# Optimization experiments

Hardware: AMD Instinct MI355X
Metric: run time of the kernel (lower is better)

## Reference

```python
import jax, jax.numpy as jnp
import numpy as np

RHO = 10.0
TAU = 0.1


def setup_inputs() -> dict:
    key = jax.random.key(0)
    k1, k2 = jax.random.split(key)
    N, D, C = 8192, 512, 128
    embeddings = jax.random.normal(k1, (N, D), dtype=jnp.float32)
    classes = jax.random.randint(k2, (N,), 0, C, dtype=jnp.int64)
    return {"embeddings": embeddings, "classes": classes}


def reference(embeddings, classes):
    n = embeddings.shape[0]
    dt = embeddings.dtype

    # calculate_similarities_pt: cosine similarity (dot products of L2-normalized embeddings)
    norms = jnp.linalg.norm(embeddings, axis=1, keepdims=True)
    normed = embeddings / jnp.maximum(norms, jnp.asarray(1e-12, dt))
    dot_products = jnp.einsum("nd,md->nm", normed, normed)  # [N, N]

    # calculate_groups_pt: same-class mask (excluding self) and different-class mask
    eq = classes[:, None] == classes[None, :]
    eye = jnp.eye(n, dtype=bool)
    same_group = (eq & ~eye).astype(dt)       # [N, N]
    different_group = (~eq).astype(dt)        # [N, N]

    # diagonal gets factor -RHO -> strongly negative score, effectively masked out
    raw_scores = ((same_group + different_group) * (1.0 + RHO) - RHO) * dot_products / TAU
    max_raw_score = jnp.max(raw_scores, axis=1, keepdims=True)
    shifted_scores = jnp.exp(raw_scores - max_raw_score)

    shifted_positive_scores = same_group * shifted_scores
    sum_shifted_negative_scores = jnp.sum(different_group * shifted_scores, axis=1, keepdims=True)

    denom = shifted_positive_scores + sum_shifted_negative_scores
    # safe_division: 0 where denominator is 0
    ratio = jnp.where(denom > 0, shifted_positive_scores / jnp.where(denom > 0, denom, 1.0), 0.0)
    # safe_log: 0 where argument is 0 (masked by same_group anyway)
    log_ratio = jnp.where(ratio > 0, jnp.log(jnp.where(ratio > 0, ratio, 1.0)), 0.0)
    infonce_losses = -log_ratio * same_group

    num_pos = jnp.sum(same_group)
    loss = jnp.where(num_pos > 0, jnp.sum(infonce_losses) / jnp.where(num_pos > 0, num_pos, 1.0), 0.0)
    return loss
```

## Files before the change

kernel.cpp:

```cpp
#include <hip/hip_runtime.h>
#include <hip/hip_bf16.h>


constexpr int   D      = 512;
constexpr int   BT     = 128;
constexpr float SHIFTL = 14.4269504088896340f;
constexpr float QS2L   = 10.0f * 1.4426950408889634f / 16129.0f;
constexpr float LN2    = 0.6931471805599453f;

typedef __attribute__((ext_vector_type(4))) int i32x4;
typedef unsigned char uchar;
typedef unsigned long ulong_t;

__device__ inline void gload_lds16(const uchar* g, void* l) {
    __builtin_amdgcn_global_load_lds(
        (const __attribute__((address_space(1))) void*)g,
        (__attribute__((address_space(3))) void*)l, 16, 0, 0);
}

__global__ void k_normalize(const float* __restrict__ emb,
                            const int* __restrict__ classes,
                            uchar* __restrict__ normed,
                            int* __restrict__ hist, int n) {
    if (blockIdx.x == 0) {
        __shared__ int h[128];
        if (threadIdx.x < 128) h[threadIdx.x] = 0;
        __syncthreads();
        for (int i = threadIdx.x; i < n; i += 256)
            atomicAdd(&h[classes[i] & 127], 1);
        __syncthreads();
        if (threadIdx.x < 128) hist[threadIdx.x] = h[threadIdx.x];
    }
    int row  = blockIdx.x * 4 + (threadIdx.x >> 6);
    int lane = threadIdx.x & 63;
    if (row >= n) return;
    const float4* src = (const float4*)(emb + (size_t)row * D);
    float4 a = src[lane * 2];
    float4 b = src[lane * 2 + 1];
    float ss = a.x*a.x + a.y*a.y + a.z*a.z + a.w*a.w
             + b.x*b.x + b.y*b.y + b.z*b.z + b.w*b.w;
#pragma unroll
    for (int m = 1; m < 64; m <<= 1) ss += __shfl_xor(ss, m, 64);
    float sc = 127.0f / fmaxf(sqrtf(ss), 1e-12f);
    union { signed char c[8]; ulong_t u; } o;
    float v[8] = {a.x, a.y, a.z, a.w, b.x, b.y, b.z, b.w};
#pragma unroll
    for (int k = 0; k < 8; ++k) {
        int q = (int)rintf(v[k] * sc);
        q = q > 127 ? 127 : (q < -127 ? -127 : q);
        o.c[k] = (signed char)q;
    }
    *(ulong_t*)&normed[(size_t)row * D + lane * 8] = o.u;
}

__global__ __launch_bounds__(256, 2) void k_zgemm(
    const uchar* __restrict__ normed, const int* __restrict__ classes,
    float* __restrict__ Zpart, int n, int nb, int npairs) {
    __shared__ char Blds[65536];
    __shared__ int clsrow[BT], clscol[BT];

    const int tid  = threadIdx.x;
    const int lane = tid & 63;
    const int w    = tid >> 6;
    const int l15  = lane & 15, l4 = lane >> 4;
    const size_t QS = (size_t)64 * n;

    int q8 = npairs >> 3, r8 = npairs & 7;
    int xcd = blockIdx.x & 7, off = blockIdx.x >> 3;
    int orig = (xcd < r8 ? xcd * (q8 + 1) : r8 * (q8 + 1) + (xcd - r8) * q8) + off;

    const int sgrid = nb >> 3;
    int idx = orig, si = 0;
    for (;;) { int rc = 36 + (sgrid - 1 - si) * 64; if (idx < rc) break; idx -= rc; ++si; }
    int bi, bj;
    if (idx < 36) { int u = 0, rem = 8; while (idx >= rem) { idx -= rem; ++u; --rem; }
                    bi = si * 8 + u; bj = si * 8 + u + idx; }
    else { idx -= 36; int sj = si + 1 + (idx >> 6); int v = idx & 63;
           bi = si * 8 + (v >> 3); bj = sj * 8 + (v & 7); }
    const int row0 = bi * BT, c0 = bj * BT;
    const bool diagblk = (bi == bj);

    if (tid < BT) clsrow[tid] = classes[row0 + tid];
    else          clscol[tid - BT] = classes[c0 + tid - BT];

    int crow[2][4];
#pragma unroll
    for (int rg = 0; rg < 2; ++rg)
#pragma unroll
        for (int r = 0; r < 4; ++r)
            crow[rg][r] = classes[row0 + w * 32 + rg * 16 + l4 * 4 + r];
    int ccv[8];
#pragma unroll
    for (int cf = 0; cf < 8; ++cf)
        ccv[cf] = classes[c0 + cf * 16 + l15];

    i32x4 areg[2][8];
#pragma unroll
    for (int rg = 0; rg < 2; ++rg)
#pragma unroll
        for (int kf = 0; kf < 8; ++kf)
            areg[rg][kf] = *(const i32x4*)&normed[
                (size_t)(row0 + w * 32 + rg * 16 + l15) * D + kf * 64 + l4 * 16];

    {
        const int colw = w * 2 + (lane >> 5);
        const int p    = lane & 31;
#pragma unroll
        for (int rr = 0; rr < 16; ++rr) {
            int col = rr * 8 + colw;
            gload_lds16(&normed[(size_t)(c0 + col) * D + ((p ^ (col & 7)) << 4)],
                        Blds + (rr * 8 + w * 2) * 512 + lane * 16);
        }
    }
    __syncthreads();

    i32x4 acc[2][8];
#pragma unroll
    for (int rg = 0; rg < 2; ++rg)
#pragma unroll
        for (int cf = 0; cf < 8; ++cf) acc[rg][cf] = (i32x4){0, 0, 0, 0};

    const int csw = l15 & 7;
#pragma unroll
    for (int kf = 0; kf < 8; ++kf) {
#pragma unroll
        for (int cf = 0; cf < 8; ++cf) {
            int cc = cf * 16 + l15;
            i32x4 bf = *(const i32x4*)(Blds + cc * 512 +
                        (((kf * 4 + l4) ^ csw) << 4));
            acc[0][cf] = __builtin_amdgcn_mfma_i32_16x16x64_i8(
                areg[0][kf], bf, acc[0][cf], 0, 0, 0);
            acc[1][cf] = __builtin_amdgcn_mfma_i32_16x16x64_i8(
                areg[1][kf], bf, acc[1][cf], 0, 0, 0);
        }
    }
    __syncthreads();

    float* redc = (float*)Blds;
    float* redr = (float*)(Blds + 8192);

    float cq[8][3];
#pragma unroll
    for (int cf = 0; cf < 8; ++cf) cq[cf][0] = cq[cf][1] = cq[cf][2] = 0.f;

#pragma unroll
    for (int rg = 0; rg < 2; ++rg) {
#pragma unroll
        for (int r = 0; r < 4; ++r) {
            int rr = w * 32 + rg * 16 + l4 * 4 + r;
            int cr = crow[rg][r];
            float z = 0.f, ns = 0.f, p1 = 0.f;
#pragma unroll
            for (int cf = 0; cf < 8; ++cf) {
                int cc = cf * 16 + l15;
                float tt = fmaf((float)acc[rg][cf][r], QS2L, -SHIFTL);
                float e = exp2f(tt);
                bool same = (cr == ccv[cf]);
                bool dg   = diagblk && (rr == cc);
                if (!same) { z += e; cq[cf][0] += e; }
                else if (!dg) { ns += tt; p1 += e; cq[cf][1] += tt; cq[cf][2] += e; }
            }
#pragma unroll
            for (int m = 1; m < 16; m <<= 1) {
                z  += __shfl_xor(z,  m, 16);
                ns += __shfl_xor(ns, m, 16);
                p1 += __shfl_xor(p1, m, 16);
            }
            if (l15 == 0) {
                redr[rr * 3 + 0] = z;
                redr[rr * 3 + 1] = ns;
                redr[rr * 3 + 2] = p1;
            }
        }
    }
    if (!diagblk) {
#pragma unroll
        for (int cf = 0; cf < 8; ++cf) {
            float z = cq[cf][0], nsv = cq[cf][1], p = cq[cf][2];
            z += __shfl_xor(z, 16, 64);  z += __shfl_xor(z, 32, 64);
            nsv += __shfl_xor(nsv, 16, 64); nsv += __shfl_xor(nsv, 32, 64);
            p += __shfl_xor(p, 16, 64);  p += __shfl_xor(p, 32, 64);
            if (l4 == 0) {
                float* pp = &redc[(w * 128 + cf * 16 + l15) * 3];
                pp[0] = z; pp[1] = nsv; pp[2] = p;
            }
        }
    }
    __syncthreads();

    if (tid < BT) {
#pragma unroll
        for (int q = 0; q < 3; ++q)
            Zpart[q * QS + (size_t)bj * n + row0 + tid] = redr[tid * 3 + q];
    } else if (!diagblk) {
        int cc = tid - BT;
#pragma unroll
        for (int q = 0; q < 3; ++q)
            Zpart[q * QS + (size_t)bi * n + c0 + cc] =
                redc[(0 * 128 + cc) * 3 + q] + redc[(1 * 128 + cc) * 3 + q] +
                redc[(2 * 128 + cc) * 3 + q] + redc[(3 * 128 + cc) * 3 + q];
    }
}

__global__ void k_rowterms(const float* __restrict__ Zpart,
                           const int* __restrict__ classes,
                           const int* __restrict__ hist,
                           float* __restrict__ rowloss,
                           float* __restrict__ rowcnt, int n) {
    int i = blockIdx.x * 256 + threadIdx.x;
    if (i >= n) return;
    const size_t QS = (size_t)64 * n;
    float z = 0.f, ns = 0.f, p1 = 0.f;
    for (int s = 0; s < 64; ++s) {
        size_t o = (size_t)s * n + i;
        z  += Zpart[o];
        ns += Zpart[QS + o];
        p1 += Zpart[2 * QS + o];
    }
    float c = (float)(hist[classes[i] & 127] - 1);
    rowloss[i] = -ns * LN2 + c * logf(z) + p1 / z;
    rowcnt[i]  = c;
}

__global__ void k_final(const float* __restrict__ rowloss,
                        const float* __restrict__ rowcnt,
                        float* __restrict__ out, int n) {
    __shared__ float sl[1024];
    __shared__ float sc[1024];
    float l = 0.f, c = 0.f;
    for (int i = threadIdx.x; i < n; i += 1024) {
        l += rowloss[i];
        c += rowcnt[i];
    }
    sl[threadIdx.x] = l;
    sc[threadIdx.x] = c;
    __syncthreads();
    for (int s = 512; s > 0; s >>= 1) {
        if (threadIdx.x < s) {
            sl[threadIdx.x] += sl[threadIdx.x + s];
            sc[threadIdx.x] += sc[threadIdx.x + s];
        }
        __syncthreads();
    }
    if (threadIdx.x == 0)
        out[0] = (sc[0] > 0.f) ? sl[0] / sc[0] : 0.f;
}

extern "C" void kernel_launch(void* const* d_in, const int* in_sizes, int n_in,
                              void* d_out, int out_size, void* d_ws, size_t ws_size,
                              hipStream_t stream) {
    const float* emb     = (const float*)d_in[0];
    const int*   classes = (const int*)d_in[1];
    float*       out     = (float*)d_out;
    const int n  = in_sizes[1];
    const int nb = n / BT;
    const int npairs = nb * (nb + 1) / 2;

    uchar*  normed  = (uchar*)d_ws;
    float*  Zpart   = (float*)((char*)d_ws + (size_t)n * D);
    float*  rowloss = Zpart + (size_t)3 * 64 * n;
    float*  rowcnt  = rowloss + n;
    int*    hist    = (int*)(rowcnt + n);

    k_normalize<<<n / 4, 256, 0, stream>>>(emb, classes, normed, hist, n);
    k_zgemm<<<npairs, 256, 0, stream>>>(normed, classes, Zpart, n, nb, npairs);
    k_rowterms<<<(n + 255) / 256, 256, 0, stream>>>(Zpart, classes, hist, rowloss, rowcnt, n);
    k_final<<<1, 1024, 0, stream>>>(rowloss, rowcnt, out, n);
}
```

Measured before the change: 86.46 us.

## Pipeline B-tile loads through a triple-buffered LDS ring over K

Replaces the single 64KB LDS load of the full B tile (all of K) with a 3-slot 16KB ring that streams K in 128-byte steps. The next stages are prefetched with async global-to-LDS loads while MFMAs run, with vmcnt waits and barriers between steps and raised wave priority around the MFMA bursts. The smaller LDS footprint allows three blocks per CU under the new launch bounds instead of two. Class labels for the epilogue are now read from the shared arrays instead of global memory. In exchange it adds barriers per step and more register pressure at the higher occupancy target.

```diff
diff --git a/kernel.cpp b/kernel.cpp
--- a/kernel.cpp
+++ b/kernel.cpp
@@ -4,6 +4,8 @@
 
 constexpr int   D      = 512;
 constexpr int   BT     = 128;
+constexpr int   BK     = 128;
+constexpr int   NSTEP  = D / BK;
 constexpr float SHIFTL = 14.4269504088896340f;
 constexpr float QS2L   = 10.0f * 1.4426950408889634f / 16129.0f;
 constexpr float LN2    = 0.6931471805599453f;
@@ -53,10 +55,10 @@
     *(ulong_t*)&normed[(size_t)row * D + lane * 8] = o.u;
 }
 
-__global__ __launch_bounds__(256, 2) void k_zgemm(
+__global__ __launch_bounds__(256, 3) void k_zgemm(
     const uchar* __restrict__ normed, const int* __restrict__ classes,
     float* __restrict__ Zpart, int n, int nb, int npairs) {
-    __shared__ char Blds[65536];
+    __shared__ char ring[3][16384];
     __shared__ int clsrow[BT], clscol[BT];
 
     const int tid  = threadIdx.x;
@@ -83,17 +85,6 @@
     if (tid < BT) clsrow[tid] = classes[row0 + tid];
     else          clscol[tid - BT] = classes[c0 + tid - BT];
 
-    int crow[2][4];
-#pragma unroll
-    for (int rg = 0; rg < 2; ++rg)
-#pragma unroll
-        for (int r = 0; r < 4; ++r)
-            crow[rg][r] = classes[row0 + w * 32 + rg * 16 + l4 * 4 + r];
-    int ccv[8];
-#pragma unroll
-    for (int cf = 0; cf < 8; ++cf)
-        ccv[cf] = classes[c0 + cf * 16 + l15];
-
     i32x4 areg[2][8];
 #pragma unroll
     for (int rg = 0; rg < 2; ++rg)
@@ -102,42 +93,86 @@
             areg[rg][kf] = *(const i32x4*)&normed[
                 (size_t)(row0 + w * 32 + rg * 16 + l15) * D + kf * 64 + l4 * 16];
 
-    {
-        const int colw = w * 2 + (lane >> 5);
-        const int p    = lane & 31;
-#pragma unroll
-        for (int rr = 0; rr < 16; ++rr) {
-            int col = rr * 8 + colw;
-            gload_lds16(&normed[(size_t)(c0 + col) * D + ((p ^ (col & 7)) << 4)],
-                        Blds + (rr * 8 + w * 2) * 512 + lane * 16);
+    const int src16 = (lane & 3) ^ ((lane >> 3) & 3);
+    size_t gB[2]; int lo[2];
+#pragma unroll
+    for (int it = 0; it < 2; ++it) {
+        int chunk = w * 2 + it;
+        int row   = chunk * 16 + (lane >> 2);
+        gB[it] = (size_t)(c0 + row) * D + src16 * 16;
+        lo[it] = chunk * 1024;
+    }
+    char* ringb = &ring[0][0];
+
+    auto STAGE = [&](int sbo, int kk) {
+#pragma unroll
+        for (int h = 0; h < 2; ++h)
+#pragma unroll
+            for (int it = 0; it < 2; ++it)
+                gload_lds16(normed + gB[it] + kk + h * 64,
+                            ringb + sbo + h * 8192 + lo[it]);
+    };
+
+    i32x4 acc[2][8];
+#pragma unroll
+    for (int rg = 0; rg < 2; ++rg)
+#pragma unroll
+        for (int cf = 0; cf < 8; ++cf) acc[rg][cf] = (i32x4){0, 0, 0, 0};
+
+    STAGE(0, 0);
+    STAGE(16384, BK);
+    __builtin_amdgcn_sched_barrier(0);
+    asm volatile("s_waitcnt vmcnt(4) lgkmcnt(0)" ::: "memory");
+    __builtin_amdgcn_s_barrier();
+    __builtin_amdgcn_sched_barrier(0);
+
+    const int rsw = (l15 >> 1) & 3;
+
+#pragma unroll
+    for (int kt = 0; kt < NSTEP; ++kt) {
+        const int cur = kt % 3;
+        if (kt + 2 < NSTEP) STAGE(((kt + 2) % 3) * 16384, (kt + 2) * BK);
+        const char* base = ringb + cur * 16384;
+#pragma unroll
+        for (int h = 0; h < 2; ++h) {
+            const char* lb = base + h * 8192;
+            i32x4 bfr[8];
+#pragma unroll
+            for (int cf = 0; cf < 8; ++cf) {
+                int rb = cf * 16 + l15;
+                bfr[cf] = *(const i32x4*)(lb + rb * 64 + ((l4 ^ rsw) << 4));
+            }
+            __builtin_amdgcn_s_setprio(1);
+#pragma unroll
+            for (int rg = 0; rg < 2; ++rg)
+#pragma unroll
+                for (int cf = 0; cf < 8; ++cf)
+                    acc[rg][cf] = __builtin_amdgcn_mfma_i32_16x16x64_i8(
+                        areg[rg][kt * 2 + h], bfr[cf], acc[rg][cf], 0, 0, 0);
+            __builtin_amdgcn_s_setprio(0);
+        }
+        __builtin_amdgcn_sched_barrier(0);
+        if (kt + 2 < NSTEP)       asm volatile("s_waitcnt vmcnt(4)" ::: "memory");
+        else if (kt + 2 == NSTEP) asm volatile("s_waitcnt vmcnt(0)" ::: "memory");
+        if (kt + 1 < NSTEP) {
+            __builtin_amdgcn_s_barrier();
+            __builtin_amdgcn_sched_barrier(0);
         }
     }
     __syncthreads();
 
-    i32x4 acc[2][8];
+    float* redr = (float*)ringb;
+    float* redc = (float*)(ringb + 2048);
+
+    int crow[2][4];
 #pragma unroll
     for (int rg = 0; rg < 2; ++rg)
 #pragma unroll
-        for (int cf = 0; cf < 8; ++cf) acc[rg][cf] = (i32x4){0, 0, 0, 0};
-
-    const int csw = l15 & 7;
-#pragma unroll
-    for (int kf = 0; kf < 8; ++kf) {
-#pragma unroll
-        for (int cf = 0; cf < 8; ++cf) {
-            int cc = cf * 16 + l15;
-            i32x4 bf = *(const i32x4*)(Blds + cc * 512 +
-                        (((kf * 4 + l4) ^ csw) << 4));
-            acc[0][cf] = __builtin_amdgcn_mfma_i32_16x16x64_i8(
-                areg[0][kf], bf, acc[0][cf], 0, 0, 0);
-            acc[1][cf] = __builtin_amdgcn_mfma_i32_16x16x64_i8(
-                areg[1][kf], bf, acc[1][cf], 0, 0, 0);
-        }
-    }
-    __syncthreads();
-
-    float* redc = (float*)Blds;
-    float* redr = (float*)(Blds + 8192);
+        for (int r = 0; r < 4; ++r)
+            crow[rg][r] = clsrow[w * 32 + rg * 16 + l4 * 4 + r];
+    int ccv[8];
+#pragma unroll
+    for (int cf = 0; cf < 8; ++cf) ccv[cf] = clscol[cf * 16 + l15];
 
     float cq[8][3];
 #pragma unroll
```

After: 75.60 us. 12.6% less time.

## Load B fragments directly from global memory instead of staging in LDS

Applied to the files above, without the earlier changes.

Drops the 64KB LDS staging of the column tile (global_load_lds plus a barrier) and has each wave read B fragments straight from global memory, relying on L1/L2 for reuse across the four waves. This frees shared memory, so launch bounds rise to 3 blocks per CU, and the per-thread class labels are read from LDS copies instead of separate global loads. The cost is four times the global/L1 traffic for B and no cooperative prefetch ahead of the MFMA loop. Higher occupancy also tightens the register budget for the large accumulator and A-fragment arrays.

```diff
diff --git a/kernel.cpp b/kernel.cpp
--- a/kernel.cpp
+++ b/kernel.cpp
@@ -11,12 +11,6 @@
 typedef __attribute__((ext_vector_type(4))) int i32x4;
 typedef unsigned char uchar;
 typedef unsigned long ulong_t;
-
-__device__ inline void gload_lds16(const uchar* g, void* l) {
-    __builtin_amdgcn_global_load_lds(
-        (const __attribute__((address_space(1))) void*)g,
-        (__attribute__((address_space(3))) void*)l, 16, 0, 0);
-}
 
 __global__ void k_normalize(const float* __restrict__ emb,
                             const int* __restrict__ classes,
@@ -53,10 +47,11 @@
     *(ulong_t*)&normed[(size_t)row * D + lane * 8] = o.u;
 }
 
-__global__ __launch_bounds__(256, 2) void k_zgemm(
+__global__ __launch_bounds__(256, 3) void k_zgemm(
     const uchar* __restrict__ normed, const int* __restrict__ classes,
     float* __restrict__ Zpart, int n, int nb, int npairs) {
-    __shared__ char Blds[65536];
+    __shared__ float redr[BT * 3];
+    __shared__ float redc[4 * BT * 3];
     __shared__ int clsrow[BT], clscol[BT];
 
     const int tid  = threadIdx.x;
@@ -83,17 +78,6 @@
     if (tid < BT) clsrow[tid] = classes[row0 + tid];
     else          clscol[tid - BT] = classes[c0 + tid - BT];
 
-    int crow[2][4];
-#pragma unroll
-    for (int rg = 0; rg < 2; ++rg)
-#pragma unroll
-        for (int r = 0; r < 4; ++r)
-            crow[rg][r] = classes[row0 + w * 32 + rg * 16 + l4 * 4 + r];
-    int ccv[8];
-#pragma unroll
-    for (int cf = 0; cf < 8; ++cf)
-        ccv[cf] = classes[c0 + cf * 16 + l15];
-
     i32x4 areg[2][8];
 #pragma unroll
     for (int rg = 0; rg < 2; ++rg)
@@ -102,42 +86,35 @@
             areg[rg][kf] = *(const i32x4*)&normed[
                 (size_t)(row0 + w * 32 + rg * 16 + l15) * D + kf * 64 + l4 * 16];
 
-    {
-        const int colw = w * 2 + (lane >> 5);
-        const int p    = lane & 31;
-#pragma unroll
-        for (int rr = 0; rr < 16; ++rr) {
-            int col = rr * 8 + colw;
-            gload_lds16(&normed[(size_t)(c0 + col) * D + ((p ^ (col & 7)) << 4)],
-                        Blds + (rr * 8 + w * 2) * 512 + lane * 16);
-        }
-    }
-    __syncthreads();
-
     i32x4 acc[2][8];
 #pragma unroll
     for (int rg = 0; rg < 2; ++rg)
 #pragma unroll
         for (int cf = 0; cf < 8; ++cf) acc[rg][cf] = (i32x4){0, 0, 0, 0};
 
-    const int csw = l15 & 7;
+    const uchar* bbase = normed + (size_t)c0 * D;
 #pragma unroll
     for (int kf = 0; kf < 8; ++kf) {
 #pragma unroll
         for (int cf = 0; cf < 8; ++cf) {
-            int cc = cf * 16 + l15;
-            i32x4 bf = *(const i32x4*)(Blds + cc * 512 +
-                        (((kf * 4 + l4) ^ csw) << 4));
+            i32x4 bf = *(const i32x4*)(bbase +
+                (size_t)(cf * 16 + l15) * D + kf * 64 + l4 * 16);
             acc[0][cf] = __builtin_amdgcn_mfma_i32_16x16x64_i8(
                 areg[0][kf], bf, acc[0][cf], 0, 0, 0);
             acc[1][cf] = __builtin_amdgcn_mfma_i32_16x16x64_i8(
                 areg[1][kf], bf, acc[1][cf], 0, 0, 0);
         }
     }
-    __syncthreads();
-
-    float* redc = (float*)Blds;
-    float* redr = (float*)(Blds + 8192);
+
+    int crow[2][4];
+#pragma unroll
+    for (int rg = 0; rg < 2; ++rg)
+#pragma unroll
+        for (int r = 0; r < 4; ++r)
+            crow[rg][r] = clsrow[w * 32 + rg * 16 + l4 * 4 + r];
+    int ccv[8];
+#pragma unroll
+    for (int cf = 0; cf < 8; ++cf) ccv[cf] = clscol[cf * 16 + l15];
 
     float cq[8][3];
 #pragma unroll
```

Result: slower. 124.6 us (+44.1%).
